# Performance work log

Measured on AMD Instinct MI355X. Metric: run time of the kernel, lower is better.

Reference implementation:

```python
import jax, jax.numpy as jnp
import numpy as np

H = 32        # num attention heads
KVH = 8       # num key/value heads
HD = 64       # head dim
D = H * HD    # hidden size 2048
EPS = 1e-6
ROPE_THETA = 10000.0
MAX_POS = 2048


def rotate_half(x):
    x1, x2 = jnp.split(x, 2, axis=-1)
    return jnp.concatenate((-x2, x1), axis=-1)


def rms_norm(x, w):
    # per-head RMSNorm over last dim, computed in fp32 like the torch module
    x32 = x.astype(jnp.float32)
    inv = jax.lax.rsqrt(jnp.mean(x32 * x32, axis=-1, keepdims=True) + EPS)
    return w * (x32 * inv).astype(x.dtype)


def setup_inputs() -> dict:
    key = jax.random.key(0)
    ks = jax.random.split(key, 6)
    B, S = 2, 2048
    hidden_states = jax.random.normal(ks[0], (B, S, D), dtype=jnp.float32)
    # rotary tables [MAX_POS, HD]
    inv_freq = 1.0 / (ROPE_THETA ** (np.arange(0, HD, 2, dtype=np.float32) / HD))
    t = np.arange(MAX_POS, dtype=np.float32)
    freqs = np.outer(t, inv_freq)                      # [MAX_POS, HD/2]
    emb = np.concatenate([freqs, freqs], axis=-1)      # [MAX_POS, HD]
    cos = jnp.asarray(np.cos(emb))
    sin = jnp.asarray(np.sin(emb))
    scale = 1.0 / np.sqrt(D)
    wq = jax.random.normal(ks[1], (D, D), dtype=jnp.float32) * scale
    wk = jax.random.normal(ks[2], (D, KVH * HD), dtype=jnp.float32) * scale
    wv = jax.random.normal(ks[3], (D, KVH * HD), dtype=jnp.float32) * scale
    wo = jax.random.normal(ks[4], (D, D), dtype=jnp.float32) * scale
    q_ln_w = jnp.ones((HD,), dtype=jnp.float32)
    k_ln_w = jnp.ones((HD,), dtype=jnp.float32)
    return {"hidden_states": hidden_states, "cos": cos, "sin": sin,
            "wq": wq, "wk": wk, "wv": wv, "wo": wo,
            "q_ln_w": q_ln_w, "k_ln_w": k_ln_w}


def reference(hidden_states, cos, sin, wq, wk, wv, wo, q_ln_w, k_ln_w):
    B, S, _ = hidden_states.shape
    n_rep = H // KVH
    q = (hidden_states @ wq).reshape(B, S, H, HD)
    k = (hidden_states @ wk).reshape(B, S, KVH, HD)
    v = (hidden_states @ wv).reshape(B, S, KVH, HD)
    # per-head RMSNorm on q/k, then to (B, heads, S, HD)
    q = rms_norm(q, q_ln_w).transpose(0, 2, 1, 3)
    k = rms_norm(k, k_ln_w).transpose(0, 2, 1, 3)
    v = v.transpose(0, 2, 1, 3)
    # RoPE
    c = cos[:S][None, None]  # [1,1,S,HD]
    s = sin[:S][None, None]
    q = q * c + rotate_half(q) * s
    k = k * c + rotate_half(k) * s
    # GQA: repeat kv heads
    k = jnp.repeat(k, n_rep, axis=1)
    v = jnp.repeat(v, n_rep, axis=1)
    scores = jnp.einsum('bhqd,bhkd->bhqk', q, k) / np.sqrt(HD)
    causal = jnp.tril(jnp.ones((S, S), dtype=bool))
    scores = jnp.where(causal, scores, -jnp.inf)
    p = jax.nn.softmax(scores.astype(jnp.float32), axis=-1).astype(q.dtype)
    out = jnp.einsum('bhqk,bhkd->bhqd', p, v)
    out = out.transpose(0, 2, 1, 3).reshape(B, S, D)
    return out @ wo
```

## Files before the change

### kernel.cpp

```cpp
#include <hip/hip_runtime.h>
#include <hip/hip_bf16.h>

#define HH 32
#define KVHN 8
#define HD 64
#define DMODEL 2048
#define SEQ 2048
#define BB 2
#define NTOK 4096
#define DKV 512
#define NQKV 3072

typedef __bf16 bf16x8 __attribute__((ext_vector_type(8)));
typedef __bf16 bf16x4 __attribute__((ext_vector_type(4)));
typedef float  f32x4  __attribute__((ext_vector_type(4)));

typedef const __attribute__((address_space(1))) void gvoid_t;
typedef __attribute__((address_space(3))) void lvoid_t;

__device__ inline void glds16(const void* g, void* l) {
  __builtin_amdgcn_global_load_lds((gvoid_t*)g, (lvoid_t*)l, 16, 0, 0);
}

__device__ inline f32x4 mfma16(bf16x8 a, bf16x8 b, f32x4 c) {
  return __builtin_amdgcn_mfma_f32_16x16x32_bf16(a, b, c, 0, 0, 0);
}

__device__ inline float fast_exp2(float x) {
  float r;
  asm("v_exp_f32 %0, %1" : "=v"(r) : "v"(x));
  return r;
}


__global__ __launch_bounds__(256)
void k_cvt_hidden(const float* __restrict__ in, __bf16* __restrict__ out) {
  int i = (blockIdx.x * 256 + threadIdx.x) * 4;
  f32x4 v = *(const f32x4*)(in + i);
  bf16x4 o;
  o[0] = (__bf16)v[0]; o[1] = (__bf16)v[1]; o[2] = (__bf16)v[2]; o[3] = (__bf16)v[3];
  *(bf16x4*)(out + i) = o;
}

__global__ __launch_bounds__(256)
void k_transpose_w(const float* __restrict__ W, __bf16* __restrict__ T, int K, int N) {
  __shared__ float tile[32][33];
  int n0 = blockIdx.x * 32, k0 = blockIdx.y * 32;
  int tx = threadIdx.x & 31, ty = threadIdx.x >> 5;
#pragma unroll
  for (int i = 0; i < 32; i += 8)
    tile[ty + i][tx] = W[(size_t)(k0 + ty + i) * N + n0 + tx];
  __syncthreads();
#pragma unroll
  for (int i = 0; i < 32; i += 8)
    T[(size_t)(n0 + ty + i) * K + k0 + tx] = (__bf16)tile[tx][ty + i];
}

__global__ __launch_bounds__(256)
void k_transpose_kv(const float* __restrict__ WK, const float* __restrict__ WV,
                    __bf16* __restrict__ T) {
  __shared__ float tile[32][33];
  const float* W = blockIdx.z ? WV : WK;
  __bf16* Td = T + (size_t)(2048 + blockIdx.z * 512) * 2048;
  int n0 = blockIdx.x * 32, k0 = blockIdx.y * 32;
  int tx = threadIdx.x & 31, ty = threadIdx.x >> 5;
#pragma unroll
  for (int i = 0; i < 32; i += 8)
    tile[ty + i][tx] = W[(size_t)(k0 + ty + i) * 512 + n0 + tx];
  __syncthreads();
#pragma unroll
  for (int i = 0; i < 32; i += 8)
    Td[(size_t)(n0 + ty + i) * 2048 + k0 + tx] = (__bf16)tile[tx][ty + i];
}

__global__ __launch_bounds__(256)
void k_transpose_v(const __bf16* __restrict__ Vt, __bf16* __restrict__ VT) {
  __shared__ __bf16 tile[32][33];
  int c0 = blockIdx.x * 32, s0 = blockIdx.y * 32, b = blockIdx.z;
  int tx = threadIdx.x & 31, ty = threadIdx.x >> 5;
#pragma unroll
  for (int i = 0; i < 32; i += 8)
    tile[ty + i][tx] = Vt[(size_t)(b * SEQ + s0 + ty + i) * DKV + c0 + tx];
  __syncthreads();
#pragma unroll
  for (int i = 0; i < 32; i += 8)
    VT[(size_t)(b * DKV + c0 + ty + i) * SEQ + s0 + tx] = tile[tx][ty + i];
}


__device__ inline void stc(float* p, float v)  { *p = v; }
__device__ inline void stc(__bf16* p, float v) { *p = (__bf16)v; }

template <int EPI, typename CT>
__global__ __launch_bounds__(256, 4)
void k_gemm3(const __bf16* __restrict__ A, const __bf16* __restrict__ BT,
             CT* __restrict__ C, int M, int N, int K,
             const float* __restrict__ cosT, const float* __restrict__ sinT,
             const float* __restrict__ qw, const float* __restrict__ kw,
             __bf16* __restrict__ Qr, __bf16* __restrict__ Kr,
             __bf16* __restrict__ Vt) {
  __shared__ alignas(16) __bf16 Al[2][128 * 32];
  __shared__ alignas(16) __bf16 Bl[2][128 * 32];
  const int tid = threadIdx.x;
  const int wid = tid >> 6, lane = tid & 63, g = lane >> 4, r16 = lane & 15;
  const int wm = wid >> 1, wn = wid & 1;
  const int nbm = M >> 7, nbn = N >> 7;
  const int nwg = nbm * nbn;
  int id = blockIdx.x;
  id = (id & 7) * (nwg >> 3) + (id >> 3);
  const int bm = id % nbm, bn = id / nbm;

  const int sr1 = tid >> 2, sr2 = 64 + (tid >> 2);
  const int c1 = (((tid & 3) ^ (sr1 & 3) ^ ((sr1 >> 2) & 3))) * 8;
  const int c2 = (((tid & 3) ^ (sr2 & 3) ^ ((sr2 >> 2) & 3))) * 8;
  const __bf16* gA1 = A + (size_t)(bm * 128 + sr1) * K + c1;
  const __bf16* gA2 = A + (size_t)(bm * 128 + sr2) * K + c2;
  const __bf16* gB1 = BT + (size_t)(bn * 128 + sr1) * K + c1;
  const __bf16* gB2 = BT + (size_t)(bn * 128 + sr2) * K + c2;

  int aoff[4], boff[4];
#pragma unroll
  for (int m = 0; m < 4; ++m) {
    int row = wm * 64 + m * 16 + r16;
    aoff[m] = row * 32 + (g ^ (row & 3) ^ ((row >> 2) & 3)) * 8;
  }
#pragma unroll
  for (int n = 0; n < 4; ++n) {
    int row = wn * 64 + n * 16 + r16;
    boff[n] = row * 32 + (g ^ (row & 3) ^ ((row >> 2) & 3)) * 8;
  }

  auto STAGE = [&](int sl, int kt) {
    const int ko = kt * 32;
    glds16(gA1 + ko, &Al[sl][tid * 8]);
    glds16(gA2 + ko, &Al[sl][2048 + tid * 8]);
    glds16(gB1 + ko, &Bl[sl][tid * 8]);
    glds16(gB2 + ko, &Bl[sl][2048 + tid * 8]);
  };

  f32x4 acc[4][4] = {};
  const int nk = K >> 5;

  STAGE(0, 0);
  for (int kt = 0; kt < nk; ++kt) {
    const int s = kt & 1;
    if (kt + 1 < nk) {
      STAGE(s ^ 1, kt + 1);
      asm volatile("s_waitcnt vmcnt(4)" ::: "memory");
    } else {
      asm volatile("s_waitcnt vmcnt(0)" ::: "memory");
    }
    __builtin_amdgcn_s_barrier();
    bf16x8 af[4], bfr[4];
#pragma unroll
    for (int m = 0; m < 4; ++m) af[m] = *(const bf16x8*)&Al[s][aoff[m]];
#pragma unroll
    for (int n = 0; n < 4; ++n) bfr[n] = *(const bf16x8*)&Bl[s][boff[n]];
    __builtin_amdgcn_s_setprio(1);
#pragma unroll
    for (int m = 0; m < 4; ++m)
#pragma unroll
      for (int n = 0; n < 4; ++n)
        acc[m][n] = mfma16(af[m], bfr[n], acc[m][n]);
    __builtin_amdgcn_s_setprio(0);
    __builtin_amdgcn_s_barrier();
  }

  if (EPI == 0) {
#pragma unroll
    for (int m = 0; m < 4; ++m) {
      int row = bm * 128 + wm * 64 + m * 16 + g * 4;
#pragma unroll
      for (int n = 0; n < 4; ++n) {
        int col = bn * 128 + wn * 64 + n * 16 + r16;
#pragma unroll
        for (int r = 0; r < 4; ++r)
          stc(&C[(size_t)(row + r) * N + col], acc[m][n][r]);
      }
    }
  } else {
    const int colbase = bn * 128 + wn * 64;
    const float QSCALE = 0.18033688011112042f;
    if (colbase < DMODEL + DKV) {
      const bool isq = colbase < DMODEL;
      const float* wp = isq ? qw : kw;
      const float qs = isq ? QSCALE : 1.0f;
      float w4[4];
#pragma unroll
      for (int n = 0; n < 4; ++n) w4[n] = wp[n * 16 + r16];
#pragma unroll
      for (int m = 0; m < 4; ++m) {
        const int rowm = bm * 128 + wm * 64 + m * 16 + g * 4;
        float ss[4];
#pragma unroll
        for (int r = 0; r < 4; ++r) {
          ss[r] = acc[m][0][r] * acc[m][0][r] + acc[m][1][r] * acc[m][1][r] +
                  acc[m][2][r] * acc[m][2][r] + acc[m][3][r] * acc[m][3][r];
#pragma unroll
          for (int mk = 1; mk < 16; mk <<= 1) ss[r] += __shfl_xor(ss[r], mk);
          ss[r] = rsqrtf(ss[r] * (1.0f / HD) + 1e-6f);
        }
#pragma unroll
        for (int r = 0; r < 4; ++r) {
          const int t = rowm + r;
          const int sidx = t & (SEQ - 1);
          const float inv_ = ss[r];
#pragma unroll
          for (int n = 0; n < 4; ++n) {
            const int d = n * 16 + r16;
            const float xn = acc[m][n][r] * inv_ * w4[n];
            const float xp = acc[m][n ^ 2][r] * inv_ * w4[n ^ 2];
            const float rot = (n < 2) ? -xp : xp;
            const float cv = cosT[sidx * HD + d], sv = sinT[sidx * HD + d];
            const float o = (xn * cv + rot * sv) * qs;
            if (isq) {
              const int hq = colbase >> 6;
              Qr[((size_t)t * HH + hq) * HD + d] = (__bf16)o;
            } else {
              const int kvh = (colbase - DMODEL) >> 6;
              Kr[((size_t)t * KVHN + kvh) * HD + d] = (__bf16)o;
            }
          }
        }
      }
    } else {
      const int vc0 = colbase - (DMODEL + DKV);
#pragma unroll
      for (int m = 0; m < 4; ++m) {
        const int rowm = bm * 128 + wm * 64 + m * 16 + g * 4;
#pragma unroll
        for (int n = 0; n < 4; ++n)
#pragma unroll
          for (int r = 0; r < 4; ++r)
            Vt[(size_t)(rowm + r) * DKV + vc0 + n * 16 + r16] = (__bf16)acc[m][n][r];
      }
    }
  }
}


__global__ __launch_bounds__(512)
void k_attn(const __bf16* __restrict__ Q, const __bf16* __restrict__ Kg,
            const __bf16* __restrict__ VT, __bf16* __restrict__ O) {
  __shared__ alignas(16) __bf16 Kl[2][64 * 64];
  __shared__ alignas(16) __bf16 Vl[2][64 * 64];
  __shared__ alignas(16) __bf16 Pl[8][16 * 72];
  const int h = blockIdx.x, b = blockIdx.z;
  const int qt = (int)gridDim.y - 1 - (int)blockIdx.y;
  const int kvh = h >> 2;
  const int tid = threadIdx.x, wid = tid >> 6, lane = tid & 63;
  const int g = lane >> 4, r16 = lane & 15;
  const int q0 = qt * 256 + wid * 32;
  __bf16* Pw = Pl[wid];

  bf16x8 qf[2][2];
#pragma unroll
  for (int rb = 0; rb < 2; ++rb)
#pragma unroll
    for (int h2 = 0; h2 < 2; ++h2)
      qf[rb][h2] = *(const bf16x8*)&Q[(((size_t)b * SEQ + q0 + rb * 16 + r16) * HH + h) * HD + h2 * 32 + g * 8];

  f32x4 acc[2][4] = {};
  float l_p[2][4] = {};

  const int rr = lane >> 3;
  const int cc = (lane & 7) ^ rr;

  auto STAGE = [&](int buf, int kb) {
    const int krow = kb * 64 + wid * 8 + rr;
    glds16(&Kg[((size_t)(b * SEQ + krow) * KVHN + kvh) * HD + cc * 8],
           &Kl[buf][wid * 512]);
    const int d = wid * 8 + rr;
    glds16(&VT[(size_t)(b * DKV + kvh * HD + d) * SEQ + (size_t)kb * 64 + cc * 8],
           &Vl[buf][wid * 512]);
  };

  const int ntile = 4 * qt + 4;
  STAGE(0, 0);
  asm volatile("s_waitcnt vmcnt(0)" ::: "memory");
  __syncthreads();

  for (int kb = 0; kb < ntile; ++kb) {
    const int cur = kb & 1;
    if (kb + 1 < ntile) STAGE(cur ^ 1, kb + 1);
    const __bf16* Kb = Kl[cur];
    const __bf16* Vb = Vl[cur];
    bf16x8 kf[4][2];
#pragma unroll
    for (int ks = 0; ks < 4; ++ks)
#pragma unroll
      for (int h2 = 0; h2 < 2; ++h2) {
        const int p = r16 + ks * 16;
        const int ch = (g + 4 * h2) ^ (p & 7);
        kf[ks][h2] = *(const bf16x8*)&Kb[p * 64 + ch * 8];
      }
#pragma unroll
    for (int rb = 0; rb < 2; ++rb) {
      const int qw = q0 + rb * 16;
      if (kb * 64 > qw + 15) continue;
      const bool needmask = (kb * 64 + 63 > qw);
      float svv[4][4];
      __builtin_amdgcn_s_setprio(1);
#pragma unroll
      for (int ks = 0; ks < 4; ++ks) {
        f32x4 sacc = {-12.f, -12.f, -12.f, -12.f};
        sacc = mfma16(qf[rb][0], kf[ks][0], sacc);
        sacc = mfma16(qf[rb][1], kf[ks][1], sacc);
#pragma unroll
        for (int r = 0; r < 4; ++r) svv[ks][r] = sacc[r];
      }
      __builtin_amdgcn_s_setprio(0);
      if (needmask) {
#pragma unroll
        for (int ks = 0; ks < 4; ++ks)
#pragma unroll
          for (int r = 0; r < 4; ++r) {
            int pg = kb * 64 + ks * 16 + r16;
            int qg = qw + g * 4 + r;
            if (pg > qg) svv[ks][r] = -1e30f;
          }
      }
#pragma unroll
      for (int ks = 0; ks < 4; ++ks)
#pragma unroll
        for (int r = 0; r < 4; ++r) {
          float p = fast_exp2(svv[ks][r]);
          l_p[rb][r] += p;
          Pw[(g * 4 + r) * 72 + ks * 16 + r16] = (__bf16)p;
        }

      bf16x8 pf0 = *(const bf16x8*)&Pw[r16 * 72 + g * 8];
      bf16x8 pf1 = *(const bf16x8*)&Pw[r16 * 72 + 32 + g * 8];
      __builtin_amdgcn_s_setprio(1);
#pragma unroll
      for (int nb = 0; nb < 4; ++nb) {
        const int d = r16 + nb * 16;
        const int ch0 = g ^ (d & 7), ch1 = (4 + g) ^ (d & 7);
        bf16x8 vf0 = *(const bf16x8*)&Vb[d * 64 + ch0 * 8];
        bf16x8 vf1 = *(const bf16x8*)&Vb[d * 64 + ch1 * 8];
        acc[rb][nb] = mfma16(pf0, vf0, acc[rb][nb]);
        acc[rb][nb] = mfma16(pf1, vf1, acc[rb][nb]);
      }
      __builtin_amdgcn_s_setprio(0);
    }
    asm volatile("s_waitcnt vmcnt(0)" ::: "memory");
    __syncthreads();
  }
#pragma unroll
  for (int rb = 0; rb < 2; ++rb) {
#pragma unroll
    for (int mk = 1; mk < 16; mk <<= 1)
#pragma unroll
      for (int r = 0; r < 4; ++r) l_p[rb][r] += __shfl_xor(l_p[rb][r], mk);
    float inv[4];
#pragma unroll
    for (int r = 0; r < 4; ++r) inv[r] = 1.0f / l_p[rb][r];
#pragma unroll
    for (int nb = 0; nb < 4; ++nb)
#pragma unroll
      for (int r = 0; r < 4; ++r)
        O[(((size_t)b * SEQ + q0 + rb * 16 + g * 4 + r) * HH + h) * HD + nb * 16 + r16] =
            (__bf16)(acc[rb][nb][r] * inv[r]);
  }
}


extern "C" void kernel_launch(void* const* d_in, const int* in_sizes, int n_in,
                              void* d_out, int out_size, void* d_ws, size_t ws_size,
                              hipStream_t stream) {
  const float* hidden = (const float*)d_in[0];
  const float* cosT   = (const float*)d_in[1];
  const float* sinT   = (const float*)d_in[2];
  const float* wq     = (const float*)d_in[3];
  const float* wk     = (const float*)d_in[4];
  const float* wv     = (const float*)d_in[5];
  const float* wo     = (const float*)d_in[6];
  const float* qw     = (const float*)d_in[7];
  const float* kw     = (const float*)d_in[8];
  float* out = (float*)d_out;
  char* ws = (char*)d_ws;

  __bf16* Abf  = (__bf16*)(ws);
  __bf16* Ob   = Abf;
  __bf16* WT   = (__bf16*)(ws + (16u << 20));
  __bf16* Qr   = (__bf16*)(ws + (28u << 20));
  __bf16* Kr   = (__bf16*)(ws + (44u << 20));
  __bf16* Vtmp = (__bf16*)(ws + (48u << 20));
  __bf16* VT   = (__bf16*)(ws + (52u << 20));
  __bf16* WoT  = (__bf16*)(ws + (56u << 20));

  k_cvt_hidden<<<8192, 256, 0, stream>>>(hidden, Abf);
  k_transpose_w<<<dim3(64, 64), 256, 0, stream>>>(wq, WT, 2048, 2048);
  k_transpose_kv<<<dim3(16, 64, 2), 256, 0, stream>>>(wk, wv, WT);
  k_transpose_w<<<dim3(64, 64), 256, 0, stream>>>(wo, WoT, 2048, 2048);

  k_gemm3<1, __bf16><<<768, 256, 0, stream>>>(Abf, WT, (__bf16*)nullptr,
      NTOK, NQKV, DMODEL, cosT, sinT, qw, kw, Qr, Kr, Vtmp);

  k_transpose_v<<<dim3(16, 64, 2), 256, 0, stream>>>(Vtmp, VT);

  k_attn<<<dim3(HH, SEQ / 256, BB), 512, 0, stream>>>(Qr, Kr, VT, Ob);

  k_gemm3<0, float><<<512, 256, 0, stream>>>(Ob, WoT, out,
      NTOK, DMODEL, DMODEL, nullptr, nullptr, nullptr, nullptr,
      nullptr, nullptr, nullptr);
}
```

Baseline: 211.5 us.

## Share V fragment loads across both row blocks and rebalance attention grid

The attention kernel now computes P for both 16-row blocks first, then loads each V fragment from LDS once and issues MFMAs for both row blocks, instead of reloading V per row block. The P scratch buffer doubles to hold both blocks. The grid is flattened to 1D, and the query-tile order is reversed for one batch and forward for the other, mixing heavy and light causal tiles. launch_bounds adds a minimum of 4 blocks, which caps registers and risks spills.

```diff
diff --git a/kernel.cpp b/kernel.cpp
--- a/kernel.cpp
+++ b/kernel.cpp
@@ -239,14 +239,17 @@
 }
 
 
-__global__ __launch_bounds__(512)
+__global__ __launch_bounds__(512, 4)
 void k_attn(const __bf16* __restrict__ Q, const __bf16* __restrict__ Kg,
             const __bf16* __restrict__ VT, __bf16* __restrict__ O) {
   __shared__ alignas(16) __bf16 Kl[2][64 * 64];
   __shared__ alignas(16) __bf16 Vl[2][64 * 64];
-  __shared__ alignas(16) __bf16 Pl[8][16 * 72];
-  const int h = blockIdx.x, b = blockIdx.z;
-  const int qt = (int)gridDim.y - 1 - (int)blockIdx.y;
+  __shared__ alignas(16) __bf16 Pl[8][32 * 72];
+  const int f = blockIdx.x;
+  const int h = f & 31;
+  const int z = (f >> 5) & 7;
+  const int b = f >> 8;
+  const int qt = b ? z : 7 - z;
   const int kvh = h >> 2;
   const int tid = threadIdx.x, wid = tid >> 6, lane = tid & 63;
   const int g = lane >> 4, r16 = lane & 15;
@@ -285,52 +288,56 @@
     if (kb + 1 < ntile) STAGE(cur ^ 1, kb + 1);
     const __bf16* Kb = Kl[cur];
     const __bf16* Vb = Vl[cur];
-    bf16x8 kf[4][2];
-#pragma unroll
-    for (int ks = 0; ks < 4; ++ks)
-#pragma unroll
-      for (int h2 = 0; h2 < 2; ++h2) {
-        const int p = r16 + ks * 16;
-        const int ch = (g + 4 * h2) ^ (p & 7);
-        kf[ks][h2] = *(const bf16x8*)&Kb[p * 64 + ch * 8];
+    const bool act0 = (kb * 64 <= q0 + 15);
+    const bool act1 = (kb * 64 <= q0 + 31);
+    if (act1) {
+      bf16x8 kf[4][2];
+#pragma unroll
+      for (int ks = 0; ks < 4; ++ks)
+#pragma unroll
+        for (int h2 = 0; h2 < 2; ++h2) {
+          const int p = r16 + ks * 16;
+          const int ch = (g + 4 * h2) ^ (p & 7);
+          kf[ks][h2] = *(const bf16x8*)&Kb[p * 64 + ch * 8];
+        }
+      bf16x8 pf[2][2];
+#pragma unroll
+      for (int rb = 0; rb < 2; ++rb) {
+        if (rb == 0 && !act0) continue;
+        const int qw = q0 + rb * 16;
+        const bool needmask = (kb * 64 + 63 > qw);
+        float svv[4][4];
+        __builtin_amdgcn_s_setprio(1);
+#pragma unroll
+        for (int ks = 0; ks < 4; ++ks) {
+          f32x4 sacc = {-12.f, -12.f, -12.f, -12.f};
+          sacc = mfma16(qf[rb][0], kf[ks][0], sacc);
+          sacc = mfma16(qf[rb][1], kf[ks][1], sacc);
+#pragma unroll
+          for (int r = 0; r < 4; ++r) svv[ks][r] = sacc[r];
+        }
+        __builtin_amdgcn_s_setprio(0);
+        if (needmask) {
+#pragma unroll
+          for (int ks = 0; ks < 4; ++ks)
+#pragma unroll
+            for (int r = 0; r < 4; ++r) {
+              int pg = kb * 64 + ks * 16 + r16;
+              int qg = qw + g * 4 + r;
+              if (pg > qg) svv[ks][r] = -1e30f;
+            }
+        }
+#pragma unroll
+        for (int ks = 0; ks < 4; ++ks)
+#pragma unroll
+          for (int r = 0; r < 4; ++r) {
+            float p = fast_exp2(svv[ks][r]);
+            l_p[rb][r] += p;
+            Pw[(rb * 16 + g * 4 + r) * 72 + ks * 16 + r16] = (__bf16)p;
+          }
+        pf[rb][0] = *(const bf16x8*)&Pw[(rb * 16 + r16) * 72 + g * 8];
+        pf[rb][1] = *(const bf16x8*)&Pw[(rb * 16 + r16) * 72 + 32 + g * 8];
       }
-#pragma unroll
-    for (int rb = 0; rb < 2; ++rb) {
-      const int qw = q0 + rb * 16;
-      if (kb * 64 > qw + 15) continue;
-      const bool needmask = (kb * 64 + 63 > qw);
-      float svv[4][4];
-      __builtin_amdgcn_s_setprio(1);
-#pragma unroll
-      for (int ks = 0; ks < 4; ++ks) {
-        f32x4 sacc = {-12.f, -12.f, -12.f, -12.f};
-        sacc = mfma16(qf[rb][0], kf[ks][0], sacc);
-        sacc = mfma16(qf[rb][1], kf[ks][1], sacc);
-#pragma unroll
-        for (int r = 0; r < 4; ++r) svv[ks][r] = sacc[r];
-      }
-      __builtin_amdgcn_s_setprio(0);
-      if (needmask) {
-#pragma unroll
-        for (int ks = 0; ks < 4; ++ks)
-#pragma unroll
-          for (int r = 0; r < 4; ++r) {
-            int pg = kb * 64 + ks * 16 + r16;
-            int qg = qw + g * 4 + r;
-            if (pg > qg) svv[ks][r] = -1e30f;
-          }
-      }
-#pragma unroll
-      for (int ks = 0; ks < 4; ++ks)
-#pragma unroll
-        for (int r = 0; r < 4; ++r) {
-          float p = fast_exp2(svv[ks][r]);
-          l_p[rb][r] += p;
-          Pw[(g * 4 + r) * 72 + ks * 16 + r16] = (__bf16)p;
-        }
-
-      bf16x8 pf0 = *(const bf16x8*)&Pw[r16 * 72 + g * 8];
-      bf16x8 pf1 = *(const bf16x8*)&Pw[r16 * 72 + 32 + g * 8];
       __builtin_amdgcn_s_setprio(1);
 #pragma unroll
       for (int nb = 0; nb < 4; ++nb) {
@@ -338,8 +345,12 @@
         const int ch0 = g ^ (d & 7), ch1 = (4 + g) ^ (d & 7);
         bf16x8 vf0 = *(const bf16x8*)&Vb[d * 64 + ch0 * 8];
         bf16x8 vf1 = *(const bf16x8*)&Vb[d * 64 + ch1 * 8];
-        acc[rb][nb] = mfma16(pf0, vf0, acc[rb][nb]);
-        acc[rb][nb] = mfma16(pf1, vf1, acc[rb][nb]);
+        if (act0) {
+          acc[0][nb] = mfma16(pf[0][0], vf0, acc[0][nb]);
+          acc[0][nb] = mfma16(pf[0][1], vf1, acc[0][nb]);
+        }
+        acc[1][nb] = mfma16(pf[1][0], vf0, acc[1][nb]);
+        acc[1][nb] = mfma16(pf[1][1], vf1, acc[1][nb]);
       }
       __builtin_amdgcn_s_setprio(0);
     }
@@ -399,7 +410,7 @@
 
   k_transpose_v<<<dim3(16, 64, 2), 256, 0, stream>>>(Vtmp, VT);
 
-  k_attn<<<dim3(HH, SEQ / 256, BB), 512, 0, stream>>>(Qr, Kr, VT, Ob);
+  k_attn<<<dim3(512), 512, 0, stream>>>(Qr, Kr, VT, Ob);
 
   k_gemm3<0, float><<<512, 256, 0, stream>>>(Ob, WoT, out,
       NTOK, DMODEL, DMODEL, nullptr, nullptr, nullptr, nullptr,
```

New measurement: 230.6 us. +9.0%, slower.

## Balance causal attention work by pairing mirrored 128-row query tiles per block

Applied to the files above, without the earlier changes.

The attention kernel now uses 128-row query tiles (16 rows per wave) and each block processes two of them, tile 15-j and then tile j, so every block does the same total number of KV tiles under the causal mask. The grid becomes a flat 512 blocks instead of 32x8x2 blocks with 256-row tiles of uneven length. This targets load imbalance and the tail from long diagonal tiles. In exchange each KV tile loaded into shared memory is reused by half as many query rows, so K/V traffic and barrier count per query row go up.

```diff
diff --git a/kernel.cpp b/kernel.cpp
--- a/kernel.cpp
+++ b/kernel.cpp
@@ -245,23 +245,14 @@
   __shared__ alignas(16) __bf16 Kl[2][64 * 64];
   __shared__ alignas(16) __bf16 Vl[2][64 * 64];
   __shared__ alignas(16) __bf16 Pl[8][16 * 72];
-  const int h = blockIdx.x, b = blockIdx.z;
-  const int qt = (int)gridDim.y - 1 - (int)blockIdx.y;
+  const int f = blockIdx.x;
+  const int b = f >> 8;
+  const int h = (f & 255) >> 3;
+  const int j = f & 7;
   const int kvh = h >> 2;
   const int tid = threadIdx.x, wid = tid >> 6, lane = tid & 63;
   const int g = lane >> 4, r16 = lane & 15;
-  const int q0 = qt * 256 + wid * 32;
   __bf16* Pw = Pl[wid];
-
-  bf16x8 qf[2][2];
-#pragma unroll
-  for (int rb = 0; rb < 2; ++rb)
-#pragma unroll
-    for (int h2 = 0; h2 < 2; ++h2)
-      qf[rb][h2] = *(const bf16x8*)&Q[(((size_t)b * SEQ + q0 + rb * 16 + r16) * HH + h) * HD + h2 * 32 + g * 8];
-
-  f32x4 acc[2][4] = {};
-  float l_p[2][4] = {};
 
   const int rr = lane >> 3;
   const int cc = (lane & 7) ^ rr;
@@ -275,92 +266,99 @@
            &Vl[buf][wid * 512]);
   };
 
-  const int ntile = 4 * qt + 4;
-  STAGE(0, 0);
-  asm volatile("s_waitcnt vmcnt(0)" ::: "memory");
-  __syncthreads();
-
-  for (int kb = 0; kb < ntile; ++kb) {
-    const int cur = kb & 1;
-    if (kb + 1 < ntile) STAGE(cur ^ 1, kb + 1);
-    const __bf16* Kb = Kl[cur];
-    const __bf16* Vb = Vl[cur];
-    bf16x8 kf[4][2];
-#pragma unroll
-    for (int ks = 0; ks < 4; ++ks)
-#pragma unroll
-      for (int h2 = 0; h2 < 2; ++h2) {
-        const int p = r16 + ks * 16;
-        const int ch = (g + 4 * h2) ^ (p & 7);
-        kf[ks][h2] = *(const bf16x8*)&Kb[p * 64 + ch * 8];
-      }
-#pragma unroll
-    for (int rb = 0; rb < 2; ++rb) {
-      const int qw = q0 + rb * 16;
-      if (kb * 64 > qw + 15) continue;
-      const bool needmask = (kb * 64 + 63 > qw);
-      float svv[4][4];
-      __builtin_amdgcn_s_setprio(1);
-#pragma unroll
-      for (int ks = 0; ks < 4; ++ks) {
-        f32x4 sacc = {-12.f, -12.f, -12.f, -12.f};
-        sacc = mfma16(qf[rb][0], kf[ks][0], sacc);
-        sacc = mfma16(qf[rb][1], kf[ks][1], sacc);
-#pragma unroll
-        for (int r = 0; r < 4; ++r) svv[ks][r] = sacc[r];
-      }
-      __builtin_amdgcn_s_setprio(0);
-      if (needmask) {
-#pragma unroll
-        for (int ks = 0; ks < 4; ++ks)
-#pragma unroll
-          for (int r = 0; r < 4; ++r) {
-            int pg = kb * 64 + ks * 16 + r16;
-            int qg = qw + g * 4 + r;
-            if (pg > qg) svv[ks][r] = -1e30f;
-          }
-      }
-#pragma unroll
-      for (int ks = 0; ks < 4; ++ks)
-#pragma unroll
-        for (int r = 0; r < 4; ++r) {
-          float p = fast_exp2(svv[ks][r]);
-          l_p[rb][r] += p;
-          Pw[(g * 4 + r) * 72 + ks * 16 + r16] = (__bf16)p;
-        }
-
-      bf16x8 pf0 = *(const bf16x8*)&Pw[r16 * 72 + g * 8];
-      bf16x8 pf1 = *(const bf16x8*)&Pw[r16 * 72 + 32 + g * 8];
-      __builtin_amdgcn_s_setprio(1);
-#pragma unroll
-      for (int nb = 0; nb < 4; ++nb) {
-        const int d = r16 + nb * 16;
-        const int ch0 = g ^ (d & 7), ch1 = (4 + g) ^ (d & 7);
-        bf16x8 vf0 = *(const bf16x8*)&Vb[d * 64 + ch0 * 8];
-        bf16x8 vf1 = *(const bf16x8*)&Vb[d * 64 + ch1 * 8];
-        acc[rb][nb] = mfma16(pf0, vf0, acc[rb][nb]);
-        acc[rb][nb] = mfma16(pf1, vf1, acc[rb][nb]);
-      }
-      __builtin_amdgcn_s_setprio(0);
-    }
+#pragma unroll 1
+  for (int phase = 0; phase < 2; ++phase) {
+    const int qt = phase ? j : 15 - j;
+    const int q0 = qt * 128 + wid * 16;
+    const int ntile = 2 * qt + 2;
+
+    bf16x8 qf[2];
+#pragma unroll
+    for (int h2 = 0; h2 < 2; ++h2)
+      qf[h2] = *(const bf16x8*)&Q[(((size_t)b * SEQ + q0 + r16) * HH + h) * HD + h2 * 32 + g * 8];
+
+    f32x4 acc[4] = {};
+    float l_p[4] = {};
+
+    STAGE(0, 0);
     asm volatile("s_waitcnt vmcnt(0)" ::: "memory");
     __syncthreads();
-  }
-#pragma unroll
-  for (int rb = 0; rb < 2; ++rb) {
+
+    for (int kb = 0; kb < ntile; ++kb) {
+      const int cur = kb & 1;
+      if (kb + 1 < ntile) STAGE(cur ^ 1, kb + 1);
+      const __bf16* Kb = Kl[cur];
+      const __bf16* Vb = Vl[cur];
+      if (kb * 64 <= q0 + 15) {
+        bf16x8 kf[4][2];
+#pragma unroll
+        for (int ks = 0; ks < 4; ++ks)
+#pragma unroll
+          for (int h2 = 0; h2 < 2; ++h2) {
+            const int p = r16 + ks * 16;
+            const int ch = (g + 4 * h2) ^ (p & 7);
+            kf[ks][h2] = *(const bf16x8*)&Kb[p * 64 + ch * 8];
+          }
+        const bool needmask = (kb * 64 + 63 > q0);
+        float svv[4][4];
+        __builtin_amdgcn_s_setprio(1);
+#pragma unroll
+        for (int ks = 0; ks < 4; ++ks) {
+          f32x4 sacc = {-12.f, -12.f, -12.f, -12.f};
+          sacc = mfma16(qf[0], kf[ks][0], sacc);
+          sacc = mfma16(qf[1], kf[ks][1], sacc);
+#pragma unroll
+          for (int r = 0; r < 4; ++r) svv[ks][r] = sacc[r];
+        }
+        __builtin_amdgcn_s_setprio(0);
+        if (needmask) {
+#pragma unroll
+          for (int ks = 0; ks < 4; ++ks)
+#pragma unroll
+            for (int r = 0; r < 4; ++r) {
+              int pg = kb * 64 + ks * 16 + r16;
+              int qg = q0 + g * 4 + r;
+              if (pg > qg) svv[ks][r] = -1e30f;
+            }
+        }
+#pragma unroll
+        for (int ks = 0; ks < 4; ++ks)
+#pragma unroll
+          for (int r = 0; r < 4; ++r) {
+            float p = fast_exp2(svv[ks][r]);
+            l_p[r] += p;
+            Pw[(g * 4 + r) * 72 + ks * 16 + r16] = (__bf16)p;
+          }
+        bf16x8 pf0 = *(const bf16x8*)&Pw[r16 * 72 + g * 8];
+        bf16x8 pf1 = *(const bf16x8*)&Pw[r16 * 72 + 32 + g * 8];
+        __builtin_amdgcn_s_setprio(1);
+#pragma unroll
+        for (int nb = 0; nb < 4; ++nb) {
+          const int d = r16 + nb * 16;
+          const int ch0 = g ^ (d & 7), ch1 = (4 + g) ^ (d & 7);
+          bf16x8 vf0 = *(const bf16x8*)&Vb[d * 64 + ch0 * 8];
+          bf16x8 vf1 = *(const bf16x8*)&Vb[d * 64 + ch1 * 8];
+          acc[nb] = mfma16(pf0, vf0, acc[nb]);
+          acc[nb] = mfma16(pf1, vf1, acc[nb]);
+        }
+        __builtin_amdgcn_s_setprio(0);
+      }
+      asm volatile("s_waitcnt vmcnt(0)" ::: "memory");
+      __syncthreads();
+    }
 #pragma unroll
     for (int mk = 1; mk < 16; mk <<= 1)
 #pragma unroll
-      for (int r = 0; r < 4; ++r) l_p[rb][r] += __shfl_xor(l_p[rb][r], mk);
+      for (int r = 0; r < 4; ++r) l_p[r] += __shfl_xor(l_p[r], mk);
     float inv[4];
 #pragma unroll
-    for (int r = 0; r < 4; ++r) inv[r] = 1.0f / l_p[rb][r];
+    for (int r = 0; r < 4; ++r) inv[r] = 1.0f / l_p[r];
 #pragma unroll
     for (int nb = 0; nb < 4; ++nb)
 #pragma unroll
       for (int r = 0; r < 4; ++r)
-        O[(((size_t)b * SEQ + q0 + rb * 16 + g * 4 + r) * HH + h) * HD + nb * 16 + r16] =
-            (__bf16)(acc[rb][nb][r] * inv[r]);
+        O[(((size_t)b * SEQ + q0 + g * 4 + r) * HH + h) * HD + nb * 16 + r16] =
+            (__bf16)(acc[nb][r] * inv[r]);
   }
 }
 
@@ -399,7 +397,7 @@
 
   k_transpose_v<<<dim3(16, 64, 2), 256, 0, stream>>>(Vtmp, VT);
 
-  k_attn<<<dim3(HH, SEQ / 256, BB), 512, 0, stream>>>(Qr, Kr, VT, Ob);
+  k_attn<<<dim3(512), 512, 0, stream>>>(Qr, Kr, VT, Ob);
 
   k_gemm3<0, float><<<512, 256, 0, stream>>>(Ob, WoT, out,
       NTOK, DMODEL, DMODEL, nullptr, nullptr, nullptr, nullptr,
```

New measurement: 201.9 us. -4.5%, faster.

## Pair causal query tiles per block and transpose score MFMA layout

Applied to the files above, without the earlier changes.

The attention grid shrinks from 512 to 256 blocks. Each block now processes two query tiles (7-j and j) in sequence so the causal work per block is balanced and a single wave of blocks covers the launch. The score MFMA swaps its operands, so each lane holds one query row. That lets P be written with packed bf16x4 stores and cuts the row-sum reduction to two shuffles. Warps whose query rows are fully masked for a K tile now skip the K fragment loads, at the cost of serialising two tiles in each block.

```diff
diff --git a/kernel.cpp b/kernel.cpp
--- a/kernel.cpp
+++ b/kernel.cpp
@@ -245,23 +245,14 @@
   __shared__ alignas(16) __bf16 Kl[2][64 * 64];
   __shared__ alignas(16) __bf16 Vl[2][64 * 64];
   __shared__ alignas(16) __bf16 Pl[8][16 * 72];
-  const int h = blockIdx.x, b = blockIdx.z;
-  const int qt = (int)gridDim.y - 1 - (int)blockIdx.y;
+  const int f = blockIdx.x;
+  const int b = f >> 7;
+  const int h = (f & 127) >> 2;
+  const int j = f & 3;
   const int kvh = h >> 2;
   const int tid = threadIdx.x, wid = tid >> 6, lane = tid & 63;
   const int g = lane >> 4, r16 = lane & 15;
-  const int q0 = qt * 256 + wid * 32;
   __bf16* Pw = Pl[wid];
-
-  bf16x8 qf[2][2];
-#pragma unroll
-  for (int rb = 0; rb < 2; ++rb)
-#pragma unroll
-    for (int h2 = 0; h2 < 2; ++h2)
-      qf[rb][h2] = *(const bf16x8*)&Q[(((size_t)b * SEQ + q0 + rb * 16 + r16) * HH + h) * HD + h2 * 32 + g * 8];
-
-  f32x4 acc[2][4] = {};
-  float l_p[2][4] = {};
 
   const int rr = lane >> 3;
   const int cc = (lane & 7) ^ rr;
@@ -275,92 +266,113 @@
            &Vl[buf][wid * 512]);
   };
 
-  const int ntile = 4 * qt + 4;
-  STAGE(0, 0);
-  asm volatile("s_waitcnt vmcnt(0)" ::: "memory");
-  __syncthreads();
-
-  for (int kb = 0; kb < ntile; ++kb) {
-    const int cur = kb & 1;
-    if (kb + 1 < ntile) STAGE(cur ^ 1, kb + 1);
-    const __bf16* Kb = Kl[cur];
-    const __bf16* Vb = Vl[cur];
-    bf16x8 kf[4][2];
-#pragma unroll
-    for (int ks = 0; ks < 4; ++ks)
-#pragma unroll
-      for (int h2 = 0; h2 < 2; ++h2) {
-        const int p = r16 + ks * 16;
-        const int ch = (g + 4 * h2) ^ (p & 7);
-        kf[ks][h2] = *(const bf16x8*)&Kb[p * 64 + ch * 8];
-      }
-#pragma unroll
-    for (int rb = 0; rb < 2; ++rb) {
-      const int qw = q0 + rb * 16;
-      if (kb * 64 > qw + 15) continue;
-      const bool needmask = (kb * 64 + 63 > qw);
-      float svv[4][4];
-      __builtin_amdgcn_s_setprio(1);
-#pragma unroll
-      for (int ks = 0; ks < 4; ++ks) {
-        f32x4 sacc = {-12.f, -12.f, -12.f, -12.f};
-        sacc = mfma16(qf[rb][0], kf[ks][0], sacc);
-        sacc = mfma16(qf[rb][1], kf[ks][1], sacc);
-#pragma unroll
-        for (int r = 0; r < 4; ++r) svv[ks][r] = sacc[r];
-      }
-      __builtin_amdgcn_s_setprio(0);
-      if (needmask) {
-#pragma unroll
-        for (int ks = 0; ks < 4; ++ks)
-#pragma unroll
-          for (int r = 0; r < 4; ++r) {
-            int pg = kb * 64 + ks * 16 + r16;
-            int qg = qw + g * 4 + r;
-            if (pg > qg) svv[ks][r] = -1e30f;
-          }
-      }
-#pragma unroll
-      for (int ks = 0; ks < 4; ++ks)
-#pragma unroll
-        for (int r = 0; r < 4; ++r) {
-          float p = fast_exp2(svv[ks][r]);
-          l_p[rb][r] += p;
-          Pw[(g * 4 + r) * 72 + ks * 16 + r16] = (__bf16)p;
-        }
-
-      bf16x8 pf0 = *(const bf16x8*)&Pw[r16 * 72 + g * 8];
-      bf16x8 pf1 = *(const bf16x8*)&Pw[r16 * 72 + 32 + g * 8];
-      __builtin_amdgcn_s_setprio(1);
-#pragma unroll
-      for (int nb = 0; nb < 4; ++nb) {
-        const int d = r16 + nb * 16;
-        const int ch0 = g ^ (d & 7), ch1 = (4 + g) ^ (d & 7);
-        bf16x8 vf0 = *(const bf16x8*)&Vb[d * 64 + ch0 * 8];
-        bf16x8 vf1 = *(const bf16x8*)&Vb[d * 64 + ch1 * 8];
-        acc[rb][nb] = mfma16(pf0, vf0, acc[rb][nb]);
-        acc[rb][nb] = mfma16(pf1, vf1, acc[rb][nb]);
-      }
-      __builtin_amdgcn_s_setprio(0);
-    }
+#pragma unroll 1
+  for (int phase = 0; phase < 2; ++phase) {
+    const int qt = phase ? j : 7 - j;
+    const int q0 = qt * 256 + wid * 32;
+    const int ntile = 4 * qt + 4;
+
+    bf16x8 qf[2][2];
+#pragma unroll
+    for (int rb = 0; rb < 2; ++rb)
+#pragma unroll
+      for (int h2 = 0; h2 < 2; ++h2)
+        qf[rb][h2] = *(const bf16x8*)&Q[(((size_t)b * SEQ + q0 + rb * 16 + r16) * HH + h) * HD + h2 * 32 + g * 8];
+
+    f32x4 acc[2][4] = {};
+    float l_q[2] = {};
+
+    STAGE(0, 0);
     asm volatile("s_waitcnt vmcnt(0)" ::: "memory");
     __syncthreads();
-  }
-#pragma unroll
-  for (int rb = 0; rb < 2; ++rb) {
-#pragma unroll
-    for (int mk = 1; mk < 16; mk <<= 1)
-#pragma unroll
-      for (int r = 0; r < 4; ++r) l_p[rb][r] += __shfl_xor(l_p[rb][r], mk);
-    float inv[4];
-#pragma unroll
-    for (int r = 0; r < 4; ++r) inv[r] = 1.0f / l_p[rb][r];
-#pragma unroll
-    for (int nb = 0; nb < 4; ++nb)
-#pragma unroll
-      for (int r = 0; r < 4; ++r)
-        O[(((size_t)b * SEQ + q0 + rb * 16 + g * 4 + r) * HH + h) * HD + nb * 16 + r16] =
-            (__bf16)(acc[rb][nb][r] * inv[r]);
+
+    for (int kb = 0; kb < ntile; ++kb) {
+      const int cur = kb & 1;
+      if (kb + 1 < ntile) STAGE(cur ^ 1, kb + 1);
+      const __bf16* Kb = Kl[cur];
+      const __bf16* Vb = Vl[cur];
+      const bool act0 = (kb * 64 <= q0 + 15);
+      const bool act1 = (kb * 64 <= q0 + 31);
+      if (act1) {
+        bf16x8 kf[4][2];
+#pragma unroll
+        for (int ks = 0; ks < 4; ++ks)
+#pragma unroll
+          for (int h2 = 0; h2 < 2; ++h2) {
+            const int p = r16 + ks * 16;
+            const int ch = (g + 4 * h2) ^ (p & 7);
+            kf[ks][h2] = *(const bf16x8*)&Kb[p * 64 + ch * 8];
+          }
+#pragma unroll
+        for (int rb = 0; rb < 2; ++rb) {
+          if (rb == 0 && !act0) continue;
+          const int qw = q0 + rb * 16;
+          const bool needmask = (kb * 64 + 63 > qw);
+          float svv[4][4];
+          __builtin_amdgcn_s_setprio(1);
+#pragma unroll
+          for (int ks = 0; ks < 4; ++ks) {
+            f32x4 sacc = {-12.f, -12.f, -12.f, -12.f};
+            sacc = mfma16(kf[ks][0], qf[rb][0], sacc);
+            sacc = mfma16(kf[ks][1], qf[rb][1], sacc);
+#pragma unroll
+            for (int r = 0; r < 4; ++r) svv[ks][r] = sacc[r];
+          }
+          __builtin_amdgcn_s_setprio(0);
+          if (needmask) {
+#pragma unroll
+            for (int ks = 0; ks < 4; ++ks)
+#pragma unroll
+              for (int r = 0; r < 4; ++r) {
+                int pg = kb * 64 + ks * 16 + g * 4 + r;
+                int qg = qw + r16;
+                if (pg > qg) svv[ks][r] = -1e30f;
+              }
+          }
+#pragma unroll
+          for (int ks = 0; ks < 4; ++ks) {
+            bf16x4 pk;
+#pragma unroll
+            for (int r = 0; r < 4; ++r) {
+              float p = fast_exp2(svv[ks][r]);
+              l_q[rb] += p;
+              pk[r] = (__bf16)p;
+            }
+            *(bf16x4*)&Pw[r16 * 72 + ks * 16 + g * 4] = pk;
+          }
+          bf16x8 pf0 = *(const bf16x8*)&Pw[r16 * 72 + g * 8];
+          bf16x8 pf1 = *(const bf16x8*)&Pw[r16 * 72 + 32 + g * 8];
+          __builtin_amdgcn_s_setprio(1);
+#pragma unroll
+          for (int nb = 0; nb < 4; ++nb) {
+            const int d = r16 + nb * 16;
+            const int ch0 = g ^ (d & 7), ch1 = (4 + g) ^ (d & 7);
+            bf16x8 vf0 = *(const bf16x8*)&Vb[d * 64 + ch0 * 8];
+            bf16x8 vf1 = *(const bf16x8*)&Vb[d * 64 + ch1 * 8];
+            acc[rb][nb] = mfma16(pf0, vf0, acc[rb][nb]);
+            acc[rb][nb] = mfma16(pf1, vf1, acc[rb][nb]);
+          }
+          __builtin_amdgcn_s_setprio(0);
+        }
+      }
+      asm volatile("s_waitcnt vmcnt(0)" ::: "memory");
+      __syncthreads();
+    }
+#pragma unroll
+    for (int rb = 0; rb < 2; ++rb) {
+      l_q[rb] += __shfl_xor(l_q[rb], 16);
+      l_q[rb] += __shfl_xor(l_q[rb], 32);
+      const float invq = 1.0f / l_q[rb];
+      float inv[4];
+#pragma unroll
+      for (int r = 0; r < 4; ++r) inv[r] = __shfl(invq, g * 4 + r);
+#pragma unroll
+      for (int nb = 0; nb < 4; ++nb)
+#pragma unroll
+        for (int r = 0; r < 4; ++r)
+          O[(((size_t)b * SEQ + q0 + rb * 16 + g * 4 + r) * HH + h) * HD + nb * 16 + r16] =
+              (__bf16)(acc[rb][nb][r] * inv[r]);
+    }
   }
 }
 
@@ -399,7 +411,7 @@
 
   k_transpose_v<<<dim3(16, 64, 2), 256, 0, stream>>>(Vtmp, VT);
 
-  k_attn<<<dim3(HH, SEQ / 256, BB), 512, 0, stream>>>(Qr, Kr, VT, Ob);
+  k_attn<<<dim3(256), 512, 0, stream>>>(Qr, Kr, VT, Ob);
 
   k_gemm3<0, float><<<512, 256, 0, stream>>>(Ob, WoT, out,
       NTOK, DMODEL, DMODEL, nullptr, nullptr, nullptr, nullptr,
```

After: 205.9 us. -2.7%, faster.
